# Performance work log

Hardware: AMD Instinct MI355X
Metric: run time of the kernel (lower is better)

Reference implementation:

```python
import jax, jax.numpy as jnp
import numpy as np
from jax import lax

SEQ_SIZE = 4096
V = 4                               # vocab size
B = 256                             # batch
FILTER_SIZES = [4, 5, 6, 7, 8]
H = 10                              # lstm hidden
I = (len(FILTER_SIZES) + 1) * V     # lstm input size = 24


def setup_inputs() -> dict:
    key = jax.random.key(0)
    ks = jax.random.split(key, 9)
    inp = {"x": jax.random.normal(ks[0], (B, 1, V * SEQ_SIZE), dtype=jnp.float32)}
    for fs in FILTER_SIZES:
        # matches nn.init.constant_(conv.weight, 0.01)
        inp[f"w{fs}"] = jnp.full((1, 1, fs), 0.01, dtype=jnp.float32)
    s = 1.0 / float(np.sqrt(H))
    shapes = {"Wih": (4 * H, I), "Whh": (4 * H, H), "bih": (4 * H,), "bhh": (4 * H,)}
    k = 1
    for d in ("f", "r"):
        for nm, sh in shapes.items():
            inp[f"{nm}_{d}"] = jax.random.uniform(ks[k], sh, jnp.float32, -s, s)
            k += 1
    return inp


def _branch(x, w, fs):
    # x: (B,1,V*S); conv1d stride=V, VALID, no bias -> (B,1,L)
    conv = lax.conv_general_dilated(x, w, window_strides=(V,), padding="VALID",
                                    dimension_numbers=("NCH", "OIH", "NCH"))
    # winner_takes_all: (x + max_over_len)^2
    m = jnp.max(conv, axis=2, keepdims=True)
    v = ((conv + m) ** 2)[:, 0, :]                                  # (B,L)
    Bsz, L = v.shape
    # shape_convolutions2 == scatter-add of v[b,i] into out[b, V*i + j], j<fs
    idx = (V * jnp.arange(L)[:, None] + jnp.arange(fs)[None, :]).reshape(-1)
    contrib = jnp.broadcast_to(v[:, :, None], (Bsz, L, fs)).reshape(Bsz, -1)
    out = jnp.zeros((Bsz, V * SEQ_SIZE), v.dtype).at[:, idx].add(contrib)
    return out.reshape(Bsz, SEQ_SIZE, V)


def _lstm_dir(xs, Wih, Whh, bih, bhh, reverse):
    # xs: (S,B,I) -> hidden states (S,B,H), aligned with input positions
    Bsz = xs.shape[1]
    h0 = jnp.zeros((Bsz, H), xs.dtype)
    c0 = jnp.zeros((Bsz, H), xs.dtype)
    b = bih + bhh

    def step(carry, xt):
        h, c = carry
        g = xt @ Wih.T + h @ Whh.T + b          # (B,4H), torch gate order i,f,g,o
        i, f, gg, o = jnp.split(g, 4, axis=1)
        c = jax.nn.sigmoid(f) * c + jax.nn.sigmoid(i) * jnp.tanh(gg)
        h = jax.nn.sigmoid(o) * jnp.tanh(c)
        return (h, c), h

    _, hs = lax.scan(step, (h0, c0), xs, reverse=reverse)
    return hs


def _forward(x, ws, Wih_f, Whh_f, bih_f, bhh_f, Wih_r, Whh_r, bih_r, bhh_r):
    Bsz = x.shape[0]
    branches = [_branch(x, w, fs) for w, fs in zip(ws, FILTER_SIZES)]
    inp_r = x.reshape(Bsz, SEQ_SIZE, V)
    l_lstmin = jnp.concatenate(branches + [inp_r], axis=2)   # (B,S,24)
    xs = jnp.swapaxes(l_lstmin, 0, 1)                        # (S,B,24)
    hf = _lstm_dir(xs, Wih_f, Whh_f, bih_f, bhh_f, False)
    hr = _lstm_dir(xs, Wih_r, Whh_r, bih_r, bhh_r, True)
    h_sum = jnp.sum(hf, axis=2) + jnp.sum(hr, axis=2)        # (S,B)
    h_sum = h_sum.T                                          # (B,S)
    # l_in * repeated h_sum, reshaped and summed over vocab == inp_r * h_sum
    l_profile = jnp.sum(inp_r * h_sum[:, :, None], axis=2)   # (B,S)
    return jax.nn.sigmoid(jnp.sum(l_profile, axis=1, keepdims=True))  # (B,1)


def reference(x, w4, w5, w6, w7, w8, Wih_f, Whh_f, bih_f, bhh_f, Wih_r, Whh_r, bih_r, bhh_r):
    return _forward(x, [w4, w5, w6, w7, w8],
                    Wih_f, Whh_f, bih_f, bhh_f, Wih_r, Whh_r, bih_r, bhh_r)
```

## Files before the change

### kernel.cpp

```cpp
#include <hip/hip_runtime.h>

#define SEQ 4096
#define NBATCH 256

__device__ __forceinline__ float sqf(float v) { return v * v; }
__device__ __forceinline__ float fexp2(float v) { return __builtin_amdgcn_exp2f(v); }
__device__ __forceinline__ float frcp(float v)  { return __builtin_amdgcn_rcpf(v); }

#define L2E 1.4426950408889634f

__device__ __forceinline__ unsigned fkey(float f) {
    const int b = __float_as_int(f);
    return (unsigned)(b ^ ((b >> 31) | 0x80000000));
}
__device__ __forceinline__ float fival(unsigned k) {
    const int b = (k & 0x80000000u) ? (int)(k ^ 0x80000000u) : (int)(~k);
    return __int_as_float(b);
}

__global__ __launch_bounds__(256) void max_kernel(
    const float* __restrict__ x,
    const float* __restrict__ w4p, const float* __restrict__ w5p,
    const float* __restrict__ w6p, const float* __restrict__ w7p,
    const float* __restrict__ w8p,
    unsigned* __restrict__ MMu)
{
    const int b    = blockIdx.x >> 2;
    const int quar = blockIdx.x & 3;
    const int tid  = threadIdx.x;
    const float* __restrict__ xr = x + (size_t)b * (4 * SEQ);

    float W4[4], W5[5], W6[6], W7[7], W8[8];
#pragma unroll
    for (int k = 0; k < 4; ++k) W4[k] = w4p[k];
#pragma unroll
    for (int k = 0; k < 5; ++k) W5[k] = w5p[k];
#pragma unroll
    for (int k = 0; k < 6; ++k) W6[k] = w6p[k];
#pragma unroll
    for (int k = 0; k < 7; ++k) W7[k] = w7p[k];
#pragma unroll
    for (int k = 0; k < 8; ++k) W8[k] = w8p[k];

    float m4 = -3.4e38f, m5 = -3.4e38f, m6 = -3.4e38f, m7 = -3.4e38f, m8 = -3.4e38f;
    for (int i = quar * (SEQ / 4) + tid; i < (quar + 1) * (SEQ / 4); i += 256) {
        const float4 t0 = *reinterpret_cast<const float4*>(xr + 4 * i);
        const float xa0 = t0.x, xa1 = t0.y, xa2 = t0.z, xa3 = t0.w;
        const float c4 = xa0 * W4[0] + xa1 * W4[1] + xa2 * W4[2] + xa3 * W4[3];
        m4 = fmaxf(m4, c4);
        if (i < SEQ - 1) {
            const float4 t1 = *reinterpret_cast<const float4*>(xr + 4 * i + 4);
            const float xa4 = t1.x, xa5 = t1.y, xa6 = t1.z, xa7 = t1.w;
            const float c5 = xa0*W5[0]+xa1*W5[1]+xa2*W5[2]+xa3*W5[3]+xa4*W5[4];
            const float c6 = xa0*W6[0]+xa1*W6[1]+xa2*W6[2]+xa3*W6[3]+xa4*W6[4]+xa5*W6[5];
            const float c7 = xa0*W7[0]+xa1*W7[1]+xa2*W7[2]+xa3*W7[3]+xa4*W7[4]+xa5*W7[5]+xa6*W7[6];
            const float c8 = xa0*W8[0]+xa1*W8[1]+xa2*W8[2]+xa3*W8[3]+xa4*W8[4]+xa5*W8[5]+xa6*W8[6]+xa7*W8[7];
            m5 = fmaxf(m5, c5); m6 = fmaxf(m6, c6);
            m7 = fmaxf(m7, c7); m8 = fmaxf(m8, c8);
        }
    }
#pragma unroll
    for (int off = 32; off; off >>= 1) {
        m4 = fmaxf(m4, __shfl_down(m4, off));
        m5 = fmaxf(m5, __shfl_down(m5, off));
        m6 = fmaxf(m6, __shfl_down(m6, off));
        m7 = fmaxf(m7, __shfl_down(m7, off));
        m8 = fmaxf(m8, __shfl_down(m8, off));
    }
    __shared__ float wr[4][5];
    if ((tid & 63) == 0) {
        const int w = tid >> 6;
        wr[w][0] = m4; wr[w][1] = m5; wr[w][2] = m6; wr[w][3] = m7; wr[w][4] = m8;
    }
    __syncthreads();
    if (tid < 5) {
        const float m = fmaxf(fmaxf(wr[0][tid], wr[1][tid]),
                              fmaxf(wr[2][tid], wr[3][tid]));
        atomicMax(&MMu[b * 5 + tid], fkey(m));
    }
}

__global__ __launch_bounds__(64) __attribute__((amdgpu_waves_per_eu(2, 2)))
void lstm_kernel(
    const float* __restrict__ x,
    const float* __restrict__ w4p, const float* __restrict__ w5p,
    const float* __restrict__ w6p, const float* __restrict__ w7p,
    const float* __restrict__ w8p,
    const unsigned* __restrict__ MMu,
    const float* __restrict__ Wih_f, const float* __restrict__ bih_f,
    const float* __restrict__ bhh_f,
    const float* __restrict__ Wih_r, const float* __restrict__ bih_r,
    const float* __restrict__ bhh_r,
    const float* __restrict__ Whh_f, const float* __restrict__ Whh_r,
    float* __restrict__ P)
{
    const int bg   = blockIdx.x & 63;
    const int d    = (blockIdx.x >> 6) & 1;
    const int q    = blockIdx.x >> 7;
    const int b0   = bg * 4;
    const int lane = threadIdx.x;

    const int s0 = q * 256 - 128;
    const int nChunks = 24, warmChunks = 8;

    __shared__ float vbuf[1024];
    __shared__ float hb[64];

    const int c  = lane >> 4;
    const int jr = lane & 15;
    const int jc = (jr < 10) ? jr : 0;

    hb[lane] = 0.f;

    const float* __restrict__ Wih = d ? Wih_r : Wih_f;
    const float* __restrict__ bi  = d ? bih_r : bih_f;
    const float* __restrict__ bh  = d ? bhh_r : bhh_f;
    float wI[13], wF[13], wG[13], wO[13];
    auto fold = [&](int g, float sc, float* w) {
        const int r = g * 10 + jc;
        const float* __restrict__ W = Wih + r * 24;
        w[0]  = (W[0] + W[1] + W[2] + W[3]) * sc;
        w[1]  = (W[4] + W[5] + W[6] + W[7]) * sc;
        w[2]  = W[4] * sc;
        w[3]  = (W[8] + W[9] + W[10] + W[11]) * sc;
        w[4]  = (W[8] + W[9]) * sc;
        w[5]  = (W[12] + W[13] + W[14] + W[15]) * sc;
        w[6]  = (W[12] + W[13] + W[14]) * sc;
        w[7]  = (W[16] + W[17] + W[18] + W[19]) * sc;
        w[8]  = W[20] * sc; w[9] = W[21] * sc;
        w[10] = W[22] * sc; w[11] = W[23] * sc;
        w[12] = (bi[r] + bh[r]) * sc;
    };
    fold(0, -L2E, wI); fold(1, -L2E, wF);
    fold(2, -2.f * L2E, wG); fold(3, -L2E, wO);

    const float* __restrict__ Whh = d ? Whh_r : Whh_f;
    float hI[10], hF[10], hG[10], hO[10];
#pragma unroll
    for (int k = 0; k < 10; ++k) {
        hI[k] = Whh[jc * 10 + k]        * (-L2E);
        hF[k] = Whh[(10 + jc) * 10 + k] * (-L2E);
        hG[k] = Whh[(20 + jc) * 10 + k] * (-2.f * L2E);
        hO[k] = Whh[(30 + jc) * 10 + k] * (-L2E);
    }
#pragma unroll
    for (int k = 0; k < 13; ++k)
        asm volatile("" : "+v"(wI[k]), "+v"(wF[k]), "+v"(wG[k]), "+v"(wO[k]));
#pragma unroll
    for (int k = 0; k < 10; ++k)
        asm volatile("" : "+v"(hI[k]), "+v"(hF[k]), "+v"(hG[k]), "+v"(hO[k]));

    const int lc = lane & 3;
    const int lr = lane >> 2;
    const float* __restrict__ xr = x + (size_t)(b0 + lc) * (4 * SEQ);

    float W4[4], W5[5], W6[6], W7[7], W8[8];
#pragma unroll
    for (int k = 0; k < 4; ++k) W4[k] = w4p[k];
#pragma unroll
    for (int k = 0; k < 5; ++k) W5[k] = w5p[k];
#pragma unroll
    for (int k = 0; k < 6; ++k) W6[k] = w6p[k];
#pragma unroll
    for (int k = 0; k < 7; ++k) W7[k] = w7p[k];
#pragma unroll
    for (int k = 0; k < 8; ++k) W8[k] = w8p[k];

    const float M4 = fival(MMu[(b0 + lc) * 5 + 0]);
    const float M5 = fival(MMu[(b0 + lc) * 5 + 1]);
    const float M6 = fival(MMu[(b0 + lc) * 5 + 2]);
    const float M7 = fival(MMu[(b0 + lc) * 5 + 3]);
    const float M8 = fival(MMu[(b0 + lc) * 5 + 4]);

    auto posof = [&](int cn) {
        int sp = s0 + cn * 16 + lr;
        if (sp < 0) sp = 0;
        return d ? (SEQ - 1 - sp) : sp;
    };
    auto loadx = [&](int pos, float4& A, float4& B, float4& C) {
        B = *reinterpret_cast<const float4*>(xr + 4 * pos);
        A = (pos > 0) ? *reinterpret_cast<const float4*>(xr + 4 * pos - 4)
                      : make_float4(0.f, 0.f, 0.f, 0.f);
        C = (pos < SEQ - 1) ? *reinterpret_cast<const float4*>(xr + 4 * pos + 4)
                            : make_float4(0.f, 0.f, 0.f, 0.f);
    };

    int posCur = posof(0);
    float4 xA, xB, xC;
    loadx(posCur, xA, xB, xC);

    float cs = 0.f, accS = 0.f;

    auto step = [&](int i) {
        const int ro = (i * 4 + c) * 4;
        const float4 q0 = *reinterpret_cast<const float4*>(&vbuf[ro]);
        const float4 q1 = *reinterpret_cast<const float4*>(&vbuf[256 + ro]);
        const float4 q2 = *reinterpret_cast<const float4*>(&vbuf[512 + ro]);
        const float  sx = vbuf[768 + ro];
        const float vv[12] = {q0.x, q0.y, q0.z, q0.w,
                              q1.x, q1.y, q1.z, q1.w,
                              q2.x, q2.y, q2.z, q2.w};
        const float4 h03 = *reinterpret_cast<const float4*>(&hb[c * 16 + 0]);
        const float4 h47 = *reinterpret_cast<const float4*>(&hb[c * 16 + 4]);
        const float2 h89 = *reinterpret_cast<const float2*>(&hb[c * 16 + 8]);
        const float hj[10] = {h03.x, h03.y, h03.z, h03.w,
                              h47.x, h47.y, h47.z, h47.w, h89.x, h89.y};
        float ei0 = wI[12], ei1 = 0.f, ef0 = wF[12], ef1 = 0.f;
        float eg0 = wG[12], eg1 = 0.f, eo0 = wO[12], eo1 = 0.f;
#pragma unroll
        for (int k = 0; k < 12; k += 2) {
            ei0 = fmaf(vv[k], wI[k], ei0); ei1 = fmaf(vv[k + 1], wI[k + 1], ei1);
            ef0 = fmaf(vv[k], wF[k], ef0); ef1 = fmaf(vv[k + 1], wF[k + 1], ef1);
            eg0 = fmaf(vv[k], wG[k], eg0); eg1 = fmaf(vv[k + 1], wG[k + 1], eg1);
            eo0 = fmaf(vv[k], wO[k], eo0); eo1 = fmaf(vv[k + 1], wO[k + 1], eo1);
        }
        const float si = ei0 + ei1, sf2 = ef0 + ef1;
        const float sg = eg0 + eg1, so2 = eo0 + eo1;
        float ai0 = si, ai1 = 0.f, af0 = sf2, af1 = 0.f;
        float ag0 = sg, ag1 = 0.f, ao0 = so2, ao1 = 0.f;
#pragma unroll
        for (int k = 0; k < 10; k += 2) {
            ai0 = fmaf(hj[k], hI[k], ai0); ai1 = fmaf(hj[k + 1], hI[k + 1], ai1);
            af0 = fmaf(hj[k], hF[k], af0); af1 = fmaf(hj[k + 1], hF[k + 1], af1);
            ag0 = fmaf(hj[k], hG[k], ag0); ag1 = fmaf(hj[k + 1], hG[k + 1], ag1);
            ao0 = fmaf(hj[k], hO[k], ao0); ao1 = fmaf(hj[k + 1], hO[k + 1], ao1);
        }
        const float eI = ai0 + ai1, eF = af0 + af1;
        const float eG = ag0 + ag1, eO = ao0 + ao1;
        const float Ai = fexp2(eI);
        const float Fv = fexp2(eF);
        const float Bg = fexp2(fminf(eG, 80.f));
        const float Ov = fexp2(eO);
        const float sf = frcp(1.f + Fv);
        const float it = fmaf(Bg, 2.f * L2E, -2.f * L2E) *
                         frcp((1.f + Ai) * (1.f + Bg));
        cs = fmaf(sf, cs, it);
        const float Dv = fexp2(fminf(cs, 80.f));
        const float hv = (1.f - Dv) * frcp((1.f + Ov) * (1.f + Dv));
        hb[c * 16 + jr] = hv;
        accS = fmaf(sx, hv, accS);
    };

    for (int cn = 0; cn < nChunks; ++cn) {
        {
            const bool okp = posCur > 0, oks = posCur < SEQ - 1;
            float xw[12];
            xw[0] = xA.x; xw[1] = xA.y; xw[2]  = xA.z; xw[3]  = xA.w;
            xw[4] = xB.x; xw[5] = xB.y; xw[6]  = xB.z; xw[7]  = xB.w;
            xw[8] = xC.x; xw[9] = xC.y; xw[10] = xC.z; xw[11] = xC.w;

            float c4s = 0.f, c5s = 0.f, c6s = 0.f, c7s = 0.f, c8s = 0.f;
            float c5p = 0.f, c6p = 0.f, c7p = 0.f, c8p = 0.f;
#pragma unroll
            for (int t = 0; t < 4; ++t) c4s += xw[4 + t] * W4[t];
#pragma unroll
            for (int t = 0; t < 5; ++t) { c5s += xw[4 + t] * W5[t]; c5p += xw[t] * W5[t]; }
#pragma unroll
            for (int t = 0; t < 6; ++t) { c6s += xw[4 + t] * W6[t]; c6p += xw[t] * W6[t]; }
#pragma unroll
            for (int t = 0; t < 7; ++t) { c7s += xw[4 + t] * W7[t]; c7p += xw[t] * W7[t]; }
#pragma unroll
            for (int t = 0; t < 8; ++t) { c8s += xw[4 + t] * W8[t]; c8p += xw[t] * W8[t]; }

            const float v4s = sqf(c4s + M4);
            const float v5s = oks ? sqf(c5s + M5) : 0.f;
            const float v6s = oks ? sqf(c6s + M6) : 0.f;
            const float v7s = oks ? sqf(c7s + M7) : 0.f;
            const float v8s = oks ? sqf(c8s + M8) : 0.f;
            const float v5p = okp ? sqf(c5p + M5) : 0.f;
            const float v6p = okp ? sqf(c6p + M6) : 0.f;
            const float v7p = okp ? sqf(c7p + M7) : 0.f;
            const float v8p = okp ? sqf(c8p + M8) : 0.f;
            const float xsum = (xw[4] + xw[5]) + (xw[6] + xw[7]);

            *reinterpret_cast<float4*>(&vbuf[lane * 4]) =
                make_float4(v4s, v5s, v5p, v6s);
            *reinterpret_cast<float4*>(&vbuf[256 + lane * 4]) =
                make_float4(v6p, v7s, v7p, v8s + v8p);
            *reinterpret_cast<float4*>(&vbuf[512 + lane * 4]) =
                make_float4(xw[4], xw[5], xw[6], xw[7]);
            vbuf[768 + lane * 4] = xsum;
        }
        asm volatile("s_waitcnt lgkmcnt(0)" ::: "memory");
        {
            const int nc = (cn + 1 < nChunks) ? cn + 1 : cn;
            posCur = posof(nc);
            loadx(posCur, xA, xB, xC);
        }
#pragma unroll 4
        for (int i = 0; i < 16; ++i) step(i);
        if (cn + 1 == warmChunks) {
            accS = 0.f;
            if (q == 0) {
                cs = 0.f;
                hb[lane] = 0.f;
            }
        }
    }

    float vA = (jr < 10) ? accS : 0.f;
#pragma unroll
    for (int off = 1; off <= 8; off <<= 1) vA += __shfl_down(vA, off);
    if (jr == 0) P[q * 512 + d * 256 + b0 + c] = vA;
}

__global__ __launch_bounds__(256) void final_kernel(const float* __restrict__ P,
                                                    float* __restrict__ out)
{
    const int b = threadIdx.x;
    float v = 0.f;
#pragma unroll
    for (int seg = 0; seg < 16; ++seg)
        v += P[seg * 512 + b] + P[seg * 512 + 256 + b];
    out[b] = frcp(1.f + fexp2(-v * L2E));
}

extern "C" void kernel_launch(void* const* d_in, const int* in_sizes, int n_in,
                              void* d_out, int out_size, void* d_ws, size_t ws_size,
                              hipStream_t stream)
{
    const float* x     = (const float*)d_in[0];
    const float* w4    = (const float*)d_in[1];
    const float* w5    = (const float*)d_in[2];
    const float* w6    = (const float*)d_in[3];
    const float* w7    = (const float*)d_in[4];
    const float* w8    = (const float*)d_in[5];
    const float* Wih_f = (const float*)d_in[6];
    const float* Whh_f = (const float*)d_in[7];
    const float* bih_f = (const float*)d_in[8];
    const float* bhh_f = (const float*)d_in[9];
    const float* Wih_r = (const float*)d_in[10];
    const float* Whh_r = (const float*)d_in[11];
    const float* bih_r = (const float*)d_in[12];
    const float* bhh_r = (const float*)d_in[13];

    float*    P   = (float*)d_ws;
    unsigned* MMu = (unsigned*)(P + 8192);

    hipMemsetAsync(MMu, 0, 1280 * sizeof(unsigned), stream);
    max_kernel<<<4 * NBATCH, 256, 0, stream>>>(x, w4, w5, w6, w7, w8, MMu);
    lstm_kernel<<<2048, 64, 0, stream>>>(x, w4, w5, w6, w7, w8, MMu,
                                         Wih_f, bih_f, bhh_f,
                                         Wih_r, bih_r, bhh_r,
                                         Whh_f, Whh_r, P);
    final_kernel<<<1, NBATCH, 0, stream>>>(P, (float*)d_out);
}
```

Measured before the change: 244.8 us.

## Hoist input-gate projection out of LSTM recurrence into per-chunk parallel precompute

Each lane now computes the full input-to-gate projections for all 40 gate rows at its own timestep, once per chunk, using pre-folded weights from a new prep kernel. It writes them to shared memory, so the serial recurrence step only adds the hidden contribution. Whh is staged through LDS in an interleaved layout, and a small prep kernel replaces the memset and folds the Wih/bias. This moves 48 FMAs per step off the sequential critical path. In exchange there are more parallel FMAs per chunk, scalar or global weight reads, a larger LDS footprint and an extra kernel launch.

```diff
diff --git a/kernel.cpp b/kernel.cpp
--- a/kernel.cpp
+++ b/kernel.cpp
@@ -16,6 +16,38 @@
 __device__ __forceinline__ float fival(unsigned k) {
     const int b = (k & 0x80000000u) ? (int)(k ^ 0x80000000u) : (int)(~k);
     return __int_as_float(b);
+}
+
+__global__ void wprep_kernel(
+    const float* __restrict__ Wih_f, const float* __restrict__ bih_f,
+    const float* __restrict__ bhh_f,
+    const float* __restrict__ Wih_r, const float* __restrict__ bih_r,
+    const float* __restrict__ bhh_r,
+    float* __restrict__ Wp, unsigned* __restrict__ MMu)
+{
+    const int t = threadIdx.x;
+    for (int i = t; i < NBATCH * 5; i += 256) MMu[i] = 0u;
+    if (t >= 80) return;
+    const int d = t / 40, r = t % 40;
+    const float* __restrict__ W  = (d ? Wih_r : Wih_f) + r * 24;
+    const float* __restrict__ bi = d ? bih_r : bih_f;
+    const float* __restrict__ bh = d ? bhh_r : bhh_f;
+    const float sc = (r >= 20 && r < 30) ? (-2.f * L2E) : (-L2E);
+    float o[13];
+    o[0]  = W[0] + W[1] + W[2] + W[3];
+    o[1]  = W[4] + W[5] + W[6] + W[7];
+    o[2]  = W[4];
+    o[3]  = W[8] + W[9] + W[10] + W[11];
+    o[4]  = W[8] + W[9];
+    o[5]  = W[12] + W[13] + W[14] + W[15];
+    o[6]  = W[12] + W[13] + W[14];
+    o[7]  = W[16] + W[17] + W[18] + W[19];
+    o[8]  = W[20]; o[9] = W[21]; o[10] = W[22]; o[11] = W[23];
+    o[12] = bi[r] + bh[r];
+    float* __restrict__ out = Wp + (d * 40 + r) * 16;
+#pragma unroll
+    for (int k = 0; k < 13; ++k) out[k] = o[k] * sc;
+    out[13] = 0.f; out[14] = 0.f; out[15] = 0.f;
 }
 
 __global__ __launch_bounds__(256) void max_kernel(
@@ -87,10 +119,7 @@
     const float* __restrict__ w6p, const float* __restrict__ w7p,
     const float* __restrict__ w8p,
     const unsigned* __restrict__ MMu,
-    const float* __restrict__ Wih_f, const float* __restrict__ bih_f,
-    const float* __restrict__ bhh_f,
-    const float* __restrict__ Wih_r, const float* __restrict__ bih_r,
-    const float* __restrict__ bhh_r,
+    const float* __restrict__ Wp,
     const float* __restrict__ Whh_f, const float* __restrict__ Whh_r,
     float* __restrict__ P)
 {
@@ -103,8 +132,9 @@
     const int s0 = q * 256 - 128;
     const int nChunks = 24, warmChunks = 8;
 
-    __shared__ float vbuf[1024];
-    __shared__ float hb[64];
+    __shared__ __align__(16) float gbuf[16 * 4 * 44];
+    __shared__ __align__(16) float hb[64];
+    __shared__ __align__(16) float wlds[400];
 
     const int c  = lane >> 4;
     const int jr = lane & 15;
@@ -112,47 +142,29 @@
 
     hb[lane] = 0.f;
 
-    const float* __restrict__ Wih = d ? Wih_r : Wih_f;
-    const float* __restrict__ bi  = d ? bih_r : bih_f;
-    const float* __restrict__ bh  = d ? bhh_r : bhh_f;
-    float wI[13], wF[13], wG[13], wO[13];
-    auto fold = [&](int g, float sc, float* w) {
-        const int r = g * 10 + jc;
-        const float* __restrict__ W = Wih + r * 24;
-        w[0]  = (W[0] + W[1] + W[2] + W[3]) * sc;
-        w[1]  = (W[4] + W[5] + W[6] + W[7]) * sc;
-        w[2]  = W[4] * sc;
-        w[3]  = (W[8] + W[9] + W[10] + W[11]) * sc;
-        w[4]  = (W[8] + W[9]) * sc;
-        w[5]  = (W[12] + W[13] + W[14] + W[15]) * sc;
-        w[6]  = (W[12] + W[13] + W[14]) * sc;
-        w[7]  = (W[16] + W[17] + W[18] + W[19]) * sc;
-        w[8]  = W[20] * sc; w[9] = W[21] * sc;
-        w[10] = W[22] * sc; w[11] = W[23] * sc;
-        w[12] = (bi[r] + bh[r]) * sc;
-    };
-    fold(0, -L2E, wI); fold(1, -L2E, wF);
-    fold(2, -2.f * L2E, wG); fold(3, -L2E, wO);
-
-    const float* __restrict__ Whh = d ? Whh_r : Whh_f;
+    {
+        const float* __restrict__ Whh = d ? Whh_r : Whh_f;
+        for (int idx = lane; idx < 400; idx += 64) {
+            const int g   = idx / 100;
+            const int rem = idx - g * 100;
+            const int u = rem / 10, k = rem - u * 10;
+            const float sc = (g == 2) ? (-2.f * L2E) : (-L2E);
+            wlds[(u * 10 + k) * 4 + g] = Whh[(g * 10 + u) * 10 + k] * sc;
+        }
+    }
+    asm volatile("s_waitcnt lgkmcnt(0)" ::: "memory");
+
     float hI[10], hF[10], hG[10], hO[10];
 #pragma unroll
     for (int k = 0; k < 10; ++k) {
-        hI[k] = Whh[jc * 10 + k]        * (-L2E);
-        hF[k] = Whh[(10 + jc) * 10 + k] * (-L2E);
-        hG[k] = Whh[(20 + jc) * 10 + k] * (-2.f * L2E);
-        hO[k] = Whh[(30 + jc) * 10 + k] * (-L2E);
-    }
-#pragma unroll
-    for (int k = 0; k < 13; ++k)
-        asm volatile("" : "+v"(wI[k]), "+v"(wF[k]), "+v"(wG[k]), "+v"(wO[k]));
-#pragma unroll
-    for (int k = 0; k < 10; ++k)
-        asm volatile("" : "+v"(hI[k]), "+v"(hF[k]), "+v"(hG[k]), "+v"(hO[k]));
+        const float4 w = *reinterpret_cast<const float4*>(&wlds[(jc * 10 + k) * 4]);
+        hI[k] = w.x; hF[k] = w.y; hG[k] = w.z; hO[k] = w.w;
+    }
 
     const int lc = lane & 3;
     const int lr = lane >> 2;
     const float* __restrict__ xr = x + (size_t)(b0 + lc) * (4 * SEQ);
+    const float* __restrict__ Wd = Wp + d * 640;
 
     float W4[4], W5[5], W6[6], W7[7], W8[8];
 #pragma unroll
@@ -189,35 +201,22 @@
     float4 xA, xB, xC;
     loadx(posCur, xA, xB, xC);
 
+    float* __restrict__ gw        = &gbuf[(lr * 4 + lc) * 44];
+    const float* __restrict__ grd = &gbuf[c * 44 + jc * 4];
+    const float* __restrict__ sxr = &gbuf[c * 44 + 40];
+
     float cs = 0.f, accS = 0.f;
 
     auto step = [&](int i) {
-        const int ro = (i * 4 + c) * 4;
-        const float4 q0 = *reinterpret_cast<const float4*>(&vbuf[ro]);
-        const float4 q1 = *reinterpret_cast<const float4*>(&vbuf[256 + ro]);
-        const float4 q2 = *reinterpret_cast<const float4*>(&vbuf[512 + ro]);
-        const float  sx = vbuf[768 + ro];
-        const float vv[12] = {q0.x, q0.y, q0.z, q0.w,
-                              q1.x, q1.y, q1.z, q1.w,
-                              q2.x, q2.y, q2.z, q2.w};
+        const float4 g4 = *reinterpret_cast<const float4*>(grd + i * 176);
+        const float  sx = sxr[i * 176];
         const float4 h03 = *reinterpret_cast<const float4*>(&hb[c * 16 + 0]);
         const float4 h47 = *reinterpret_cast<const float4*>(&hb[c * 16 + 4]);
         const float2 h89 = *reinterpret_cast<const float2*>(&hb[c * 16 + 8]);
         const float hj[10] = {h03.x, h03.y, h03.z, h03.w,
                               h47.x, h47.y, h47.z, h47.w, h89.x, h89.y};
-        float ei0 = wI[12], ei1 = 0.f, ef0 = wF[12], ef1 = 0.f;
-        float eg0 = wG[12], eg1 = 0.f, eo0 = wO[12], eo1 = 0.f;
-#pragma unroll
-        for (int k = 0; k < 12; k += 2) {
-            ei0 = fmaf(vv[k], wI[k], ei0); ei1 = fmaf(vv[k + 1], wI[k + 1], ei1);
-            ef0 = fmaf(vv[k], wF[k], ef0); ef1 = fmaf(vv[k + 1], wF[k + 1], ef1);
-            eg0 = fmaf(vv[k], wG[k], eg0); eg1 = fmaf(vv[k + 1], wG[k + 1], eg1);
-            eo0 = fmaf(vv[k], wO[k], eo0); eo1 = fmaf(vv[k + 1], wO[k + 1], eo1);
-        }
-        const float si = ei0 + ei1, sf2 = ef0 + ef1;
-        const float sg = eg0 + eg1, so2 = eo0 + eo1;
-        float ai0 = si, ai1 = 0.f, af0 = sf2, af1 = 0.f;
-        float ag0 = sg, ag1 = 0.f, ao0 = so2, ao1 = 0.f;
+        float ai0 = g4.x, ai1 = 0.f, af0 = g4.y, af1 = 0.f;
+        float ag0 = g4.z, ag1 = 0.f, ao0 = g4.w, ao1 = 0.f;
 #pragma unroll
         for (int k = 0; k < 10; k += 2) {
             ai0 = fmaf(hj[k], hI[k], ai0); ai1 = fmaf(hj[k + 1], hI[k + 1], ai1);
@@ -242,6 +241,7 @@
     };
 
     for (int cn = 0; cn < nChunks; ++cn) {
+        float vv[12], xsum;
         {
             const bool okp = posCur > 0, oks = posCur < SEQ - 1;
             float xw[12];
@@ -262,24 +262,39 @@
 #pragma unroll
             for (int t = 0; t < 8; ++t) { c8s += xw[4 + t] * W8[t]; c8p += xw[t] * W8[t]; }
 
-            const float v4s = sqf(c4s + M4);
-            const float v5s = oks ? sqf(c5s + M5) : 0.f;
-            const float v6s = oks ? sqf(c6s + M6) : 0.f;
-            const float v7s = oks ? sqf(c7s + M7) : 0.f;
+            vv[0]  = sqf(c4s + M4);
+            vv[1]  = oks ? sqf(c5s + M5) : 0.f;
+            vv[2]  = okp ? sqf(c5p + M5) : 0.f;
+            vv[3]  = oks ? sqf(c6s + M6) : 0.f;
+            vv[4]  = okp ? sqf(c6p + M6) : 0.f;
+            vv[5]  = oks ? sqf(c7s + M7) : 0.f;
+            vv[6]  = okp ? sqf(c7p + M7) : 0.f;
             const float v8s = oks ? sqf(c8s + M8) : 0.f;
-            const float v5p = okp ? sqf(c5p + M5) : 0.f;
-            const float v6p = okp ? sqf(c6p + M6) : 0.f;
-            const float v7p = okp ? sqf(c7p + M7) : 0.f;
             const float v8p = okp ? sqf(c8p + M8) : 0.f;
-            const float xsum = (xw[4] + xw[5]) + (xw[6] + xw[7]);
-
-            *reinterpret_cast<float4*>(&vbuf[lane * 4]) =
-                make_float4(v4s, v5s, v5p, v6s);
-            *reinterpret_cast<float4*>(&vbuf[256 + lane * 4]) =
-                make_float4(v6p, v7s, v7p, v8s + v8p);
-            *reinterpret_cast<float4*>(&vbuf[512 + lane * 4]) =
-                make_float4(xw[4], xw[5], xw[6], xw[7]);
-            vbuf[768 + lane * 4] = xsum;
+            vv[7]  = v8s + v8p;
+            vv[8]  = xw[4]; vv[9] = xw[5]; vv[10] = xw[6]; vv[11] = xw[7];
+            xsum   = (xw[4] + xw[5]) + (xw[6] + xw[7]);
+        }
+        {
+            float a[40];
+#pragma unroll
+            for (int g = 0; g < 4; ++g)
+#pragma unroll
+                for (int u = 0; u < 10; ++u) {
+                    const float* __restrict__ R = Wd + (g * 10 + u) * 16;
+                    float a0 = R[12], a1 = 0.f;
+#pragma unroll
+                    for (int k = 0; k < 12; k += 2) {
+                        a0 = fmaf(vv[k],     R[k],     a0);
+                        a1 = fmaf(vv[k + 1], R[k + 1], a1);
+                    }
+                    a[g * 10 + u] = a0 + a1;
+                }
+#pragma unroll
+            for (int u = 0; u < 10; ++u)
+                *reinterpret_cast<float4*>(&gw[u * 4]) =
+                    make_float4(a[u], a[10 + u], a[20 + u], a[30 + u]);
+            gw[40] = xsum;
         }
         asm volatile("s_waitcnt lgkmcnt(0)" ::: "memory");
         {
@@ -336,12 +351,12 @@
 
     float*    P   = (float*)d_ws;
     unsigned* MMu = (unsigned*)(P + 8192);
-
-    hipMemsetAsync(MMu, 0, 1280 * sizeof(unsigned), stream);
+    float*    Wpp = (float*)(MMu + 1280);
+
+    wprep_kernel<<<1, 256, 0, stream>>>(Wih_f, bih_f, bhh_f,
+                                        Wih_r, bih_r, bhh_r, Wpp, MMu);
     max_kernel<<<4 * NBATCH, 256, 0, stream>>>(x, w4, w5, w6, w7, w8, MMu);
     lstm_kernel<<<2048, 64, 0, stream>>>(x, w4, w5, w6, w7, w8, MMu,
-                                         Wih_f, bih_f, bhh_f,
-                                         Wih_r, bih_r, bhh_r,
-                                         Whh_f, Whh_r, P);
+                                         Wpp, Whh_f, Whh_r, P);
     final_kernel<<<1, NBATCH, 0, stream>>>(P, (float*)d_out);
 }
```

After: 275.2 us. 1.12x slower.

## Pack LSTM gate FMAs into float2 vectors and drop memset/atomic max

Applied to the files above, without the earlier changes.

Packs the gate weights into two-wide float vectors (I/F and G/O pairs) so the compiler can emit packed FMA instructions, roughly halving the FMA instruction count in the serial recurrence. The max kernel now writes per-quarter partial maxima directly instead of using atomicMax on order-preserving keys. This removes the memset launch, and the LSTM kernel combines the four partials itself. Register-pinning asm barriers move inside the chunk loop to keep weights resident, which may raise register pressure.

```diff
diff --git a/kernel.cpp b/kernel.cpp
--- a/kernel.cpp
+++ b/kernel.cpp
@@ -2,28 +2,21 @@
 
 #define SEQ 4096
 #define NBATCH 256
+
+typedef float v2f __attribute__((ext_vector_type(2)));
 
 __device__ __forceinline__ float sqf(float v) { return v * v; }
 __device__ __forceinline__ float fexp2(float v) { return __builtin_amdgcn_exp2f(v); }
 __device__ __forceinline__ float frcp(float v)  { return __builtin_amdgcn_rcpf(v); }
 
 #define L2E 1.4426950408889634f
-
-__device__ __forceinline__ unsigned fkey(float f) {
-    const int b = __float_as_int(f);
-    return (unsigned)(b ^ ((b >> 31) | 0x80000000));
-}
-__device__ __forceinline__ float fival(unsigned k) {
-    const int b = (k & 0x80000000u) ? (int)(k ^ 0x80000000u) : (int)(~k);
-    return __int_as_float(b);
-}
 
 __global__ __launch_bounds__(256) void max_kernel(
     const float* __restrict__ x,
     const float* __restrict__ w4p, const float* __restrict__ w5p,
     const float* __restrict__ w6p, const float* __restrict__ w7p,
     const float* __restrict__ w8p,
-    unsigned* __restrict__ MMu)
+    float* __restrict__ Mq)
 {
     const int b    = blockIdx.x >> 2;
     const int quar = blockIdx.x & 3;
@@ -76,7 +69,7 @@
     if (tid < 5) {
         const float m = fmaxf(fmaxf(wr[0][tid], wr[1][tid]),
                               fmaxf(wr[2][tid], wr[3][tid]));
-        atomicMax(&MMu[b * 5 + tid], fkey(m));
+        Mq[blockIdx.x * 5 + tid] = m;
     }
 }
 
@@ -86,7 +79,7 @@
     const float* __restrict__ w4p, const float* __restrict__ w5p,
     const float* __restrict__ w6p, const float* __restrict__ w7p,
     const float* __restrict__ w8p,
-    const unsigned* __restrict__ MMu,
+    const float* __restrict__ Mq,
     const float* __restrict__ Wih_f, const float* __restrict__ bih_f,
     const float* __restrict__ bhh_f,
     const float* __restrict__ Wih_r, const float* __restrict__ bih_r,
@@ -134,21 +127,22 @@
     fold(0, -L2E, wI); fold(1, -L2E, wF);
     fold(2, -2.f * L2E, wG); fold(3, -L2E, wO);
 
+    v2f wIF[13], wGO[13];
+#pragma unroll
+    for (int k = 0; k < 13; ++k) {
+        wIF[k] = (v2f){wI[k], wF[k]};
+        wGO[k] = (v2f){wG[k], wO[k]};
+    }
+
     const float* __restrict__ Whh = d ? Whh_r : Whh_f;
-    float hI[10], hF[10], hG[10], hO[10];
+    v2f hIF[10], hGO[10];
 #pragma unroll
     for (int k = 0; k < 10; ++k) {
-        hI[k] = Whh[jc * 10 + k]        * (-L2E);
-        hF[k] = Whh[(10 + jc) * 10 + k] * (-L2E);
-        hG[k] = Whh[(20 + jc) * 10 + k] * (-2.f * L2E);
-        hO[k] = Whh[(30 + jc) * 10 + k] * (-L2E);
-    }
-#pragma unroll
-    for (int k = 0; k < 13; ++k)
-        asm volatile("" : "+v"(wI[k]), "+v"(wF[k]), "+v"(wG[k]), "+v"(wO[k]));
-#pragma unroll
-    for (int k = 0; k < 10; ++k)
-        asm volatile("" : "+v"(hI[k]), "+v"(hF[k]), "+v"(hG[k]), "+v"(hO[k]));
+        hIF[k] = (v2f){Whh[jc * 10 + k]        * (-L2E),
+                       Whh[(10 + jc) * 10 + k] * (-L2E)};
+        hGO[k] = (v2f){Whh[(20 + jc) * 10 + k] * (-2.f * L2E),
+                       Whh[(30 + jc) * 10 + k] * (-L2E)};
+    }
 
     const int lc = lane & 3;
     const int lr = lane >> 2;
@@ -166,11 +160,12 @@
 #pragma unroll
     for (int k = 0; k < 8; ++k) W8[k] = w8p[k];
 
-    const float M4 = fival(MMu[(b0 + lc) * 5 + 0]);
-    const float M5 = fival(MMu[(b0 + lc) * 5 + 1]);
-    const float M6 = fival(MMu[(b0 + lc) * 5 + 2]);
-    const float M7 = fival(MMu[(b0 + lc) * 5 + 3]);
-    const float M8 = fival(MMu[(b0 + lc) * 5 + 4]);
+    const float* __restrict__ Mb = Mq + (size_t)(b0 + lc) * 20;
+    float M4 = fmaxf(fmaxf(Mb[0],  Mb[5]),  fmaxf(Mb[10], Mb[15]));
+    float M5 = fmaxf(fmaxf(Mb[1],  Mb[6]),  fmaxf(Mb[11], Mb[16]));
+    float M6 = fmaxf(fmaxf(Mb[2],  Mb[7]),  fmaxf(Mb[12], Mb[17]));
+    float M7 = fmaxf(fmaxf(Mb[3],  Mb[8]),  fmaxf(Mb[13], Mb[18]));
+    float M8 = fmaxf(fmaxf(Mb[4],  Mb[9]),  fmaxf(Mb[14], Mb[19]));
 
     auto posof = [&](int cn) {
         int sp = s0 + cn * 16 + lr;
@@ -205,32 +200,29 @@
         const float2 h89 = *reinterpret_cast<const float2*>(&hb[c * 16 + 8]);
         const float hj[10] = {h03.x, h03.y, h03.z, h03.w,
                               h47.x, h47.y, h47.z, h47.w, h89.x, h89.y};
-        float ei0 = wI[12], ei1 = 0.f, ef0 = wF[12], ef1 = 0.f;
-        float eg0 = wG[12], eg1 = 0.f, eo0 = wO[12], eo1 = 0.f;
+        v2f eIF0 = wIF[12], eIF1 = (v2f){0.f, 0.f};
+        v2f eGO0 = wGO[12], eGO1 = (v2f){0.f, 0.f};
 #pragma unroll
         for (int k = 0; k < 12; k += 2) {
-            ei0 = fmaf(vv[k], wI[k], ei0); ei1 = fmaf(vv[k + 1], wI[k + 1], ei1);
-            ef0 = fmaf(vv[k], wF[k], ef0); ef1 = fmaf(vv[k + 1], wF[k + 1], ef1);
-            eg0 = fmaf(vv[k], wG[k], eg0); eg1 = fmaf(vv[k + 1], wG[k + 1], eg1);
-            eo0 = fmaf(vv[k], wO[k], eo0); eo1 = fmaf(vv[k + 1], wO[k + 1], eo1);
-        }
-        const float si = ei0 + ei1, sf2 = ef0 + ef1;
-        const float sg = eg0 + eg1, so2 = eo0 + eo1;
-        float ai0 = si, ai1 = 0.f, af0 = sf2, af1 = 0.f;
-        float ag0 = sg, ag1 = 0.f, ao0 = so2, ao1 = 0.f;
+            const v2f v0 = (v2f){vv[k], vv[k]};
+            const v2f v1 = (v2f){vv[k + 1], vv[k + 1]};
+            eIF0 += v0 * wIF[k]; eIF1 += v1 * wIF[k + 1];
+            eGO0 += v0 * wGO[k]; eGO1 += v1 * wGO[k + 1];
+        }
+        v2f aIF0 = eIF0 + eIF1, aIF1 = (v2f){0.f, 0.f};
+        v2f aGO0 = eGO0 + eGO1, aGO1 = (v2f){0.f, 0.f};
 #pragma unroll
         for (int k = 0; k < 10; k += 2) {
-            ai0 = fmaf(hj[k], hI[k], ai0); ai1 = fmaf(hj[k + 1], hI[k + 1], ai1);
-            af0 = fmaf(hj[k], hF[k], af0); af1 = fmaf(hj[k + 1], hF[k + 1], af1);
-            ag0 = fmaf(hj[k], hG[k], ag0); ag1 = fmaf(hj[k + 1], hG[k + 1], ag1);
-            ao0 = fmaf(hj[k], hO[k], ao0); ao1 = fmaf(hj[k + 1], hO[k + 1], ao1);
-        }
-        const float eI = ai0 + ai1, eF = af0 + af1;
-        const float eG = ag0 + ag1, eO = ao0 + ao1;
-        const float Ai = fexp2(eI);
-        const float Fv = fexp2(eF);
-        const float Bg = fexp2(fminf(eG, 80.f));
-        const float Ov = fexp2(eO);
+            const v2f h0 = (v2f){hj[k], hj[k]};
+            const v2f h1 = (v2f){hj[k + 1], hj[k + 1]};
+            aIF0 += h0 * hIF[k]; aIF1 += h1 * hIF[k + 1];
+            aGO0 += h0 * hGO[k]; aGO1 += h1 * hGO[k + 1];
+        }
+        const v2f eIF = aIF0 + aIF1, eGO = aGO0 + aGO1;
+        const float Ai = fexp2(eIF.x);
+        const float Fv = fexp2(eIF.y);
+        const float Bg = fexp2(fminf(eGO.x, 80.f));
+        const float Ov = fexp2(eGO.y);
         const float sf = frcp(1.f + Fv);
         const float it = fmaf(Bg, 2.f * L2E, -2.f * L2E) *
                          frcp((1.f + Ai) * (1.f + Bg));
@@ -242,6 +234,34 @@
     };
 
     for (int cn = 0; cn < nChunks; ++cn) {
+        asm volatile("" :
+            "+v"(wIF[0]), "+v"(wIF[1]), "+v"(wIF[2]), "+v"(wIF[3]),
+            "+v"(wIF[4]), "+v"(wIF[5]), "+v"(wIF[6]), "+v"(wIF[7]),
+            "+v"(wIF[8]), "+v"(wIF[9]), "+v"(wIF[10]), "+v"(wIF[11]),
+            "+v"(wIF[12]),
+            "+v"(wGO[0]), "+v"(wGO[1]), "+v"(wGO[2]), "+v"(wGO[3]),
+            "+v"(wGO[4]), "+v"(wGO[5]), "+v"(wGO[6]), "+v"(wGO[7]),
+            "+v"(wGO[8]), "+v"(wGO[9]), "+v"(wGO[10]), "+v"(wGO[11]),
+            "+v"(wGO[12]));
+        asm volatile("" :
+            "+v"(hIF[0]), "+v"(hIF[1]), "+v"(hIF[2]), "+v"(hIF[3]),
+            "+v"(hIF[4]), "+v"(hIF[5]), "+v"(hIF[6]), "+v"(hIF[7]),
+            "+v"(hIF[8]), "+v"(hIF[9]),
+            "+v"(hGO[0]), "+v"(hGO[1]), "+v"(hGO[2]), "+v"(hGO[3]),
+            "+v"(hGO[4]), "+v"(hGO[5]), "+v"(hGO[6]), "+v"(hGO[7]),
+            "+v"(hGO[8]), "+v"(hGO[9]));
+        asm volatile("" :
+            "+v"(W4[0]), "+v"(W4[1]), "+v"(W4[2]), "+v"(W4[3]),
+            "+v"(W5[0]), "+v"(W5[1]), "+v"(W5[2]), "+v"(W5[3]), "+v"(W5[4]),
+            "+v"(W6[0]), "+v"(W6[1]), "+v"(W6[2]), "+v"(W6[3]), "+v"(W6[4]),
+            "+v"(W6[5]),
+            "+v"(W7[0]), "+v"(W7[1]), "+v"(W7[2]), "+v"(W7[3]), "+v"(W7[4]),
+            "+v"(W7[5]), "+v"(W7[6]),
+            "+v"(W8[0]), "+v"(W8[1]), "+v"(W8[2]), "+v"(W8[3]), "+v"(W8[4]),
+            "+v"(W8[5]), "+v"(W8[6]), "+v"(W8[7]));
+        asm volatile("" :
+            "+v"(M4), "+v"(M5), "+v"(M6), "+v"(M7), "+v"(M8));
+
         {
             const bool okp = posCur > 0, oks = posCur < SEQ - 1;
             float xw[12];
@@ -334,12 +354,11 @@
     const float* bih_r = (const float*)d_in[12];
     const float* bhh_r = (const float*)d_in[13];
 
-    float*    P   = (float*)d_ws;
-    unsigned* MMu = (unsigned*)(P + 8192);
-
-    hipMemsetAsync(MMu, 0, 1280 * sizeof(unsigned), stream);
-    max_kernel<<<4 * NBATCH, 256, 0, stream>>>(x, w4, w5, w6, w7, w8, MMu);
-    lstm_kernel<<<2048, 64, 0, stream>>>(x, w4, w5, w6, w7, w8, MMu,
+    float* P  = (float*)d_ws;
+    float* Mq = P + 8192;
+
+    max_kernel<<<4 * NBATCH, 256, 0, stream>>>(x, w4, w5, w6, w7, w8, Mq);
+    lstm_kernel<<<2048, 64, 0, stream>>>(x, w4, w5, w6, w7, w8, Mq,
                                          Wih_f, bih_f, bhh_f,
                                          Wih_r, bih_r, bhh_r,
                                          Whh_f, Whh_r, P);
```

Result: faster. 237.6 us (-2.9%).
